# Optimization experiments

Measured on AMD Instinct MI355X. Metric: run time of the kernel, lower is better.

The kernel has to match this reference:

```python
import jax, jax.numpy as jnp
import numpy as np

DIM = 768
N_HEADS = 12
HEAD_DIM = DIM // N_HEADS
SCALE = HEAD_DIM ** -0.5


def setup_inputs() -> dict:
    key = jax.random.key(0)
    ks = jax.random.split(key, 5)
    B, N = 8, 1024
    x = jax.random.normal(ks[0], (B, N, DIM), dtype=jnp.float32)
    # Linear weights stored as (in, out) for x @ W; torch stores (out, in).
    w_qkv = jax.random.normal(ks[1], (DIM, 3 * DIM), dtype=jnp.float32) * (DIM ** -0.5)
    b_qkv = jnp.zeros((3 * DIM,), dtype=jnp.float32)
    w_proj = jax.random.normal(ks[2], (DIM, DIM), dtype=jnp.float32) * (DIM ** -0.5)
    b_proj = jnp.zeros((DIM,), dtype=jnp.float32)
    return {"x": x, "w_qkv": w_qkv, "b_qkv": b_qkv, "w_proj": w_proj, "b_proj": b_proj}


def reference(x, w_qkv, b_qkv, w_proj, b_proj):
    B, N, _ = x.shape
    qkv = x @ w_qkv + b_qkv                       # [B, N, 3*dim]
    qkv = qkv.reshape(B, N, 3, N_HEADS, HEAD_DIM)
    qkv = jnp.transpose(qkv, (2, 0, 3, 1, 4))     # [3, B, H, N, hd]
    q, k, v = qkv[0], qkv[1], qkv[2]
    attn = jnp.einsum("bhqd,bhkd->bhqk", q, k) * SCALE
    attn = jax.nn.softmax(attn, axis=-1)
    out = jnp.einsum("bhqk,bhkd->bhqd", attn, v)  # [B, H, N, hd]
    out = jnp.transpose(out, (0, 2, 1, 3)).reshape(B, N, DIM)
    return out @ w_proj + b_proj
```

## Files before the change

### kernel.cpp

```cpp
#include <hip/hip_runtime.h>
#include <cstdint>

#define DIM 768
#define NH 12
#define HD 64
#define SEQ 1024
#define NBH 96

#define QOFF  ((size_t)0)
#define KOFF  ((size_t)6291456)
#define VOFF  ((size_t)12582912)
#define AOFF  ((size_t)18874368)
#define XOFF  ((size_t)25165824)
#define WQOFF ((size_t)31457280)
#define WPOFF ((size_t)33226752)

#define QSCALE 0.18033688f

typedef __attribute__((ext_vector_type(8))) __bf16 bf16x8;
typedef __attribute__((ext_vector_type(4))) float f32x4;
typedef unsigned short u16;

__device__ __forceinline__ u16 f2bf(float f) {
    union { float f; unsigned u; } x; x.f = f;
    unsigned r = x.u + 0x7fffu + ((x.u >> 16) & 1u);
    return (u16)(r >> 16);
}

__device__ __forceinline__ void async_cp16(const void* g, void* l) {
    __builtin_amdgcn_global_load_lds((const __attribute__((address_space(1))) void*)g,
                                     (__attribute__((address_space(3))) void*)l, 16, 0, 0);
}

__global__ __launch_bounds__(256) void conv_x(const float* __restrict__ in, u16* __restrict__ out) {
    int i = blockIdx.x * 256 + threadIdx.x;
    float4 v = *(const float4*)&in[(size_t)i * 4];
    ushort4 o; o.x = f2bf(v.x); o.y = f2bf(v.y); o.z = f2bf(v.z); o.w = f2bf(v.w);
    *(ushort4*)&out[(size_t)i * 4] = o;
}

__global__ __launch_bounds__(256) void conv_t(const float* __restrict__ w, u16* __restrict__ wt,
                                              int N, int K) {
    __shared__ float T[64][65];
    const int k0 = blockIdx.y * 64, n0 = blockIdx.x * 64;
    const int tid = threadIdx.x;
    const int r = tid >> 4, c4 = (tid & 15) * 4;
#pragma unroll
    for (int i = 0; i < 4; ++i) {
        float4 v = *(const float4*)&w[(size_t)(k0 + r + 16 * i) * N + n0 + c4];
        T[r + 16 * i][c4 + 0] = v.x; T[r + 16 * i][c4 + 1] = v.y;
        T[r + 16 * i][c4 + 2] = v.z; T[r + 16 * i][c4 + 3] = v.w;
    }
    __syncthreads();
#pragma unroll
    for (int i = 0; i < 4; ++i) {
        int rr = r + 16 * i;
        ushort4 o;
        o.x = f2bf(T[c4 + 0][rr]); o.y = f2bf(T[c4 + 1][rr]);
        o.z = f2bf(T[c4 + 2][rr]); o.w = f2bf(T[c4 + 3][rr]);
        *(ushort4*)&wt[(size_t)(n0 + rr) * K + k0 + c4] = o;
    }
}

template <int EPI>
__global__ __launch_bounds__(256) void gemm_bt(const u16* __restrict__ A,
                                               const u16* __restrict__ Bt,
                                               const float* __restrict__ bias,
                                               float* __restrict__ outf,
                                               u16* __restrict__ outq) {
    __shared__ __align__(16) u16 As[128 * 64];
    __shared__ __align__(16) u16 Bs[128 * 64];
    const int tid = threadIdx.x;
    const int lane = tid & 63;
    const int w = tid >> 6;
    const int wm = w >> 1, wn = w & 1;
    const int m0 = blockIdx.y * 128, n0 = blockIdx.x * 128;

    const int lgrp = lane >> 3;
    const int gg = (lane & 7) ^ lgrp;
    const u16* ga = A  + (size_t)(m0 + w * 32 + lgrp) * 768 + gg * 8;
    const u16* gb = Bt + (size_t)(n0 + w * 32 + lgrp) * 768 + gg * 8;
    u16* lba = As + w * 4 * 512;
    u16* lbb = Bs + w * 4 * 512;

    const int l15 = lane & 15, qg = lane >> 4, q4 = qg * 4;

    int aoff[4][2], boff[4][2];
#pragma unroll
    for (int r = 0; r < 4; ++r) {
        int row = 64 * wm + 16 * r + l15;
#pragma unroll
        for (int kc = 0; kc < 2; ++kc)
            aoff[r][kc] = row * 64 + (((4 * kc + qg) ^ (row & 7)) << 3);
    }
#pragma unroll
    for (int c = 0; c < 4; ++c) {
        int row = 64 * wn + 16 * c + l15;
#pragma unroll
        for (int kc = 0; kc < 2; ++kc)
            boff[c][kc] = row * 64 + (((4 * kc + qg) ^ (row & 7)) << 3);
    }

    f32x4 acc[4][4] = {};

    for (int k0 = 0; k0 < 768; k0 += 64) {
#pragma unroll
        for (int i = 0; i < 4; ++i) {
            async_cp16(ga + (size_t)i * 8 * 768 + k0, lba + i * 512);
            async_cp16(gb + (size_t)i * 8 * 768 + k0, lbb + i * 512);
        }
        __syncthreads();
        bf16x8 af[4][2], bfr[4][2];
#pragma unroll
        for (int r = 0; r < 4; ++r)
#pragma unroll
            for (int kc = 0; kc < 2; ++kc) af[r][kc] = *(const bf16x8*)&As[aoff[r][kc]];
#pragma unroll
        for (int c = 0; c < 4; ++c)
#pragma unroll
            for (int kc = 0; kc < 2; ++kc) bfr[c][kc] = *(const bf16x8*)&Bs[boff[c][kc]];
#pragma unroll
        for (int kc = 0; kc < 2; ++kc)
#pragma unroll
            for (int r = 0; r < 4; ++r)
#pragma unroll
                for (int c = 0; c < 4; ++c)
                    acc[r][c] = __builtin_amdgcn_mfma_f32_16x16x32_bf16(af[r][kc], bfr[c][kc], acc[r][c], 0, 0, 0);
        __syncthreads();
    }

#pragma unroll
    for (int r = 0; r < 4; ++r) {
#pragma unroll
        for (int c = 0; c < 4; ++c) {
            const int cg = n0 + 64 * wn + 16 * c + l15;
            const float bv = bias[cg];
            const int mb = m0 + 64 * wm + 16 * r + q4;
            if constexpr (EPI == 0) {
#pragma unroll
                for (int g = 0; g < 4; ++g)
                    outf[(size_t)(mb + g) * DIM + cg] = acc[r][c][g] + bv;
            } else {
                const int which = (cg >= 1536) ? 2 : (cg >= 768 ? 1 : 0);
                const int rem = cg - which * 768;
                const int h = rem >> 6, d = rem & 63;
                const int b = mb >> 10, q = mb & 1023;
                if (which == 0) {
#pragma unroll
                    for (int g = 0; g < 4; ++g)
                        outq[QOFF + ((size_t)(b * NH + h) * SEQ + q + g) * HD + d] =
                            f2bf((acc[r][c][g] + bv) * QSCALE);
                } else if (which == 1) {
#pragma unroll
                    for (int g = 0; g < 4; ++g)
                        outq[KOFF + ((size_t)(b * NH + h) * SEQ + q + g) * HD + d] =
                            f2bf(acc[r][c][g] + bv);
                } else {
                    ushort4 pk;
                    pk.x = f2bf(acc[r][c][0] + bv); pk.y = f2bf(acc[r][c][1] + bv);
                    pk.z = f2bf(acc[r][c][2] + bv); pk.w = f2bf(acc[r][c][3] + bv);
                    *(ushort4*)&outq[VOFF + ((size_t)(b * NH + h) * HD + d) * SEQ + q] = pk;
                }
            }
        }
    }
}

__global__ __launch_bounds__(256) void flash_attn(const u16* __restrict__ ws, u16* __restrict__ attn_out) {
    __shared__ __align__(16) u16 Ks[64 * 72];
    __shared__ __align__(16) u16 Vs[64 * 72];
    __shared__ __align__(16) u16 Ps[128 * 72];

    const int tid = threadIdx.x;
    const int lane = tid & 63;
    const int wv = tid >> 6;
    const int qt = blockIdx.x;
    const int bh = blockIdx.y;
    const u16* qp = ws + QOFF + (size_t)bh * SEQ * HD;
    const u16* kp = ws + KOFF + (size_t)bh * SEQ * HD;
    const u16* vp = ws + VOFF + (size_t)bh * HD * SEQ;

    const int l15 = lane & 15, qg = lane >> 4, q8 = qg * 8, q4 = qg * 4;

    bf16x8 bq[2][2];
#pragma unroll
    for (int r = 0; r < 2; ++r)
#pragma unroll
        for (int kc = 0; kc < 2; ++kc)
            bq[r][kc] = *(const bf16x8*)&qp[(size_t)(qt * 128 + 32 * wv + 16 * r + l15) * HD + 32 * kc + q8];

    f32x4 oacc[2][4] = {};
    float lsum[2] = {0.f, 0.f};

    for (int kt = 0; kt < 16; ++kt) {
        __syncthreads();
#pragma unroll
        for (int i = 0; i < 2; ++i) {
            int off = (tid + 256 * i) * 8;
            int row = off >> 6, col = off & 63;
            *(uint4*)&Ks[row * 72 + col] = *(const uint4*)&kp[(size_t)(kt * 64 + row) * HD + col];
            *(uint4*)&Vs[row * 72 + col] = *(const uint4*)&vp[(size_t)row * SEQ + kt * 64 + col];
        }
        __syncthreads();

        f32x4 st[4][2] = {};
#pragma unroll
        for (int c = 0; c < 4; ++c) {
#pragma unroll
            for (int kc = 0; kc < 2; ++kc) {
                bf16x8 ak = *(const bf16x8*)&Ks[(16 * c + l15) * 72 + 32 * kc + q8];
#pragma unroll
                for (int r = 0; r < 2; ++r)
                    st[c][r] = __builtin_amdgcn_mfma_f32_16x16x32_bf16(ak, bq[r][kc], st[c][r], 0, 0, 0);
            }
        }

#pragma unroll
        for (int r = 0; r < 2; ++r) {
#pragma unroll
            for (int c = 0; c < 4; ++c) {
                float p0 = __builtin_amdgcn_exp2f(st[c][r][0]);
                float p1 = __builtin_amdgcn_exp2f(st[c][r][1]);
                float p2 = __builtin_amdgcn_exp2f(st[c][r][2]);
                float p3 = __builtin_amdgcn_exp2f(st[c][r][3]);
                lsum[r] += (p0 + p1) + (p2 + p3);
                ushort4 pk; pk.x = f2bf(p0); pk.y = f2bf(p1); pk.z = f2bf(p2); pk.w = f2bf(p3);
                *(ushort4*)&Ps[(32 * wv + 16 * r + l15) * 72 + 16 * c + q4] = pk;
            }
        }

#pragma unroll
        for (int r = 0; r < 2; ++r) {
#pragma unroll
            for (int kc = 0; kc < 2; ++kc) {
                bf16x8 ap = *(const bf16x8*)&Ps[(32 * wv + 16 * r + l15) * 72 + 32 * kc + q8];
#pragma unroll
                for (int cd = 0; cd < 4; ++cd) {
                    bf16x8 bv = *(const bf16x8*)&Vs[(16 * cd + l15) * 72 + 32 * kc + q8];
                    oacc[r][cd] = __builtin_amdgcn_mfma_f32_16x16x32_bf16(ap, bv, oacc[r][cd], 0, 0, 0);
                }
            }
        }
    }

#pragma unroll
    for (int r = 0; r < 2; ++r) {
        lsum[r] += __shfl_xor(lsum[r], 16);
        lsum[r] += __shfl_xor(lsum[r], 32);
    }
    float linv[2][4];
#pragma unroll
    for (int r = 0; r < 2; ++r)
#pragma unroll
        for (int g = 0; g < 4; ++g)
            linv[r][g] = 1.f / __shfl(lsum[r], q4 + g);

    const int b = bh / NH, h = bh % NH;
#pragma unroll
    for (int r = 0; r < 2; ++r) {
#pragma unroll
        for (int g = 0; g < 4; ++g) {
            int qrow = qt * 128 + 32 * wv + 16 * r + q4 + g;
            size_t grow = (size_t)(b * SEQ + qrow) * DIM + h * HD;
#pragma unroll
            for (int cd = 0; cd < 4; ++cd)
                attn_out[grow + 16 * cd + l15] = f2bf(oacc[r][cd][g] * linv[r][g]);
        }
    }
}

extern "C" void kernel_launch(void* const* d_in, const int* in_sizes, int n_in,
                              void* d_out, int out_size, void* d_ws, size_t ws_size,
                              hipStream_t stream) {
    const float* x      = (const float*)d_in[0];
    const float* w_qkv  = (const float*)d_in[1];
    const float* b_qkv  = (const float*)d_in[2];
    const float* w_proj = (const float*)d_in[3];
    const float* b_proj = (const float*)d_in[4];
    float* out = (float*)d_out;
    u16* ws = (u16*)d_ws;

    conv_x<<<6144, 256, 0, stream>>>(x, ws + XOFF);
    conv_t<<<dim3(36, 12), 256, 0, stream>>>(w_qkv, ws + WQOFF, 2304, 768);
    conv_t<<<dim3(12, 12), 256, 0, stream>>>(w_proj, ws + WPOFF, 768, 768);
    gemm_bt<1><<<dim3(18, 64), 256, 0, stream>>>(ws + XOFF, ws + WQOFF, b_qkv, nullptr, ws);
    flash_attn<<<dim3(8, 96), 256, 0, stream>>>(ws, ws + AOFF);
    gemm_bt<0><<<dim3(6, 64), 256, 0, stream>>>(ws + AOFF, ws + WPOFF, b_proj, out, nullptr);
}
```

Before: 212.3 us.

## Double-buffer GEMM LDS tiles with async prefetch and merge prep kernels

The GEMM kernel now uses two LDS buffers and issues async global-to-LDS loads two k-steps ahead, using explicit vmcnt waits and barriers so loads overlap with MFMA compute. The three conversion kernels (x cast and two weight transposes) are merged into one launch to cut launch overhead. The change doubles LDS use per block, which may lower occupancy, and it relies on hand-coded waitcnt encodings being correct.

```diff
diff --git a/kernel.cpp b/kernel.cpp
--- a/kernel.cpp
+++ b/kernel.cpp
@@ -17,6 +17,12 @@
 
 #define QSCALE 0.18033688f
 
+#define WAIT_VM8   __builtin_amdgcn_s_waitcnt(0x0F78)
+#define WAIT_VM0   __builtin_amdgcn_s_waitcnt(0x0F70)
+#define WAIT_LGKM0 __builtin_amdgcn_s_waitcnt(0xC07F)
+#define BAR        __builtin_amdgcn_s_barrier()
+#define CFENCE     __asm__ __volatile__("" ::: "memory")
+
 typedef __attribute__((ext_vector_type(8))) __bf16 bf16x8;
 typedef __attribute__((ext_vector_type(4))) float f32x4;
 typedef unsigned short u16;
@@ -32,18 +38,25 @@
                                      (__attribute__((address_space(3))) void*)l, 16, 0, 0);
 }
 
-__global__ __launch_bounds__(256) void conv_x(const float* __restrict__ in, u16* __restrict__ out) {
-    int i = blockIdx.x * 256 + threadIdx.x;
-    float4 v = *(const float4*)&in[(size_t)i * 4];
-    ushort4 o; o.x = f2bf(v.x); o.y = f2bf(v.y); o.z = f2bf(v.z); o.w = f2bf(v.w);
-    *(ushort4*)&out[(size_t)i * 4] = o;
-}
-
-__global__ __launch_bounds__(256) void conv_t(const float* __restrict__ w, u16* __restrict__ wt,
-                                              int N, int K) {
+__global__ __launch_bounds__(256) void prep(const float* __restrict__ x,
+                                            const float* __restrict__ wq,
+                                            const float* __restrict__ wp,
+                                            u16* __restrict__ ws) {
+    const int bid = blockIdx.x;
+    const int tid = threadIdx.x;
+    if (bid < 6144) {
+        int i = bid * 256 + tid;
+        float4 v = *(const float4*)&x[(size_t)i * 4];
+        ushort4 o; o.x = f2bf(v.x); o.y = f2bf(v.y); o.z = f2bf(v.z); o.w = f2bf(v.w);
+        *(ushort4*)&ws[XOFF + (size_t)i * 4] = o;
+        return;
+    }
     __shared__ float T[64][65];
-    const int k0 = blockIdx.y * 64, n0 = blockIdx.x * 64;
-    const int tid = threadIdx.x;
+    const float* w; u16* wt; int N, bx, by;
+    if (bid < 6576) { int b = bid - 6144; w = wq; wt = ws + WQOFF; N = 2304; bx = b % 36; by = b / 36; }
+    else            { int b = bid - 6576; w = wp; wt = ws + WPOFF; N = 768;  bx = b % 12; by = b / 12; }
+    const int K = 768;
+    const int k0 = by * 64, n0 = bx * 64;
     const int r = tid >> 4, c4 = (tid & 15) * 4;
 #pragma unroll
     for (int i = 0; i < 4; ++i) {
@@ -68,8 +81,8 @@
                                                const float* __restrict__ bias,
                                                float* __restrict__ outf,
                                                u16* __restrict__ outq) {
-    __shared__ __align__(16) u16 As[128 * 64];
-    __shared__ __align__(16) u16 Bs[128 * 64];
+    __shared__ __align__(16) u16 As[2][128 * 64];
+    __shared__ __align__(16) u16 Bs[2][128 * 64];
     const int tid = threadIdx.x;
     const int lane = tid & 63;
     const int w = tid >> 6;
@@ -80,8 +93,6 @@
     const int gg = (lane & 7) ^ lgrp;
     const u16* ga = A  + (size_t)(m0 + w * 32 + lgrp) * 768 + gg * 8;
     const u16* gb = Bt + (size_t)(n0 + w * 32 + lgrp) * 768 + gg * 8;
-    u16* lba = As + w * 4 * 512;
-    u16* lbb = Bs + w * 4 * 512;
 
     const int l15 = lane & 15, qg = lane >> 4, q4 = qg * 4;
 
@@ -101,24 +112,39 @@
             boff[c][kc] = row * 64 + (((4 * kc + qg) ^ (row & 7)) << 3);
     }
 
+#define ISSUE(buf, kk)                                                          \
+    {                                                                           \
+        _Pragma("unroll")                                                       \
+        for (int i = 0; i < 4; ++i) {                                           \
+            async_cp16(ga + (size_t)i * 8 * 768 + (kk), &As[buf][w * 2048 + i * 512]); \
+            async_cp16(gb + (size_t)i * 8 * 768 + (kk), &Bs[buf][w * 2048 + i * 512]); \
+        }                                                                       \
+    }
+
+    ISSUE(0, 0)
+    ISSUE(1, 64)
+
     f32x4 acc[4][4] = {};
 
-    for (int k0 = 0; k0 < 768; k0 += 64) {
-#pragma unroll
-        for (int i = 0; i < 4; ++i) {
-            async_cp16(ga + (size_t)i * 8 * 768 + k0, lba + i * 512);
-            async_cp16(gb + (size_t)i * 8 * 768 + k0, lbb + i * 512);
-        }
-        __syncthreads();
+#pragma unroll
+    for (int k = 0; k < 12; ++k) {
+        const int cur = k & 1;
+        if (k < 11) { WAIT_VM8; } else { WAIT_VM0; }
+        BAR;
+        CFENCE;
         bf16x8 af[4][2], bfr[4][2];
 #pragma unroll
         for (int r = 0; r < 4; ++r)
 #pragma unroll
-            for (int kc = 0; kc < 2; ++kc) af[r][kc] = *(const bf16x8*)&As[aoff[r][kc]];
+            for (int kc = 0; kc < 2; ++kc) af[r][kc] = *(const bf16x8*)&As[cur][aoff[r][kc]];
 #pragma unroll
         for (int c = 0; c < 4; ++c)
 #pragma unroll
-            for (int kc = 0; kc < 2; ++kc) bfr[c][kc] = *(const bf16x8*)&Bs[boff[c][kc]];
+            for (int kc = 0; kc < 2; ++kc) bfr[c][kc] = *(const bf16x8*)&Bs[cur][boff[c][kc]];
+        WAIT_LGKM0;
+        CFENCE;
+        BAR;
+        if (k + 2 < 12) ISSUE(cur, (k + 2) * 64)
 #pragma unroll
         for (int kc = 0; kc < 2; ++kc)
 #pragma unroll
@@ -126,8 +152,8 @@
 #pragma unroll
                 for (int c = 0; c < 4; ++c)
                     acc[r][c] = __builtin_amdgcn_mfma_f32_16x16x32_bf16(af[r][kc], bfr[c][kc], acc[r][c], 0, 0, 0);
-        __syncthreads();
-    }
+    }
+#undef ISSUE
 
 #pragma unroll
     for (int r = 0; r < 4; ++r) {
@@ -280,9 +306,7 @@
     float* out = (float*)d_out;
     u16* ws = (u16*)d_ws;
 
-    conv_x<<<6144, 256, 0, stream>>>(x, ws + XOFF);
-    conv_t<<<dim3(36, 12), 256, 0, stream>>>(w_qkv, ws + WQOFF, 2304, 768);
-    conv_t<<<dim3(12, 12), 256, 0, stream>>>(w_proj, ws + WPOFF, 768, 768);
+    prep<<<6720, 256, 0, stream>>>(x, w_qkv, w_proj, ws);
     gemm_bt<1><<<dim3(18, 64), 256, 0, stream>>>(ws + XOFF, ws + WQOFF, b_qkv, nullptr, ws);
     flash_attn<<<dim3(8, 96), 256, 0, stream>>>(ws, ws + AOFF);
     gemm_bt<0><<<dim3(6, 64), 256, 0, stream>>>(ws + AOFF, ws + WPOFF, b_proj, out, nullptr);
```

Result: slower. 216.7 us (+2.0%).
